# Optimization experiments

Measured on AMD Instinct MI355X. Metric: run time of the kernel, lower is better.

The kernel has to match this reference:

```python
import jax, jax.numpy as jnp
import numpy as np

NEG_SLOPE = 0.2

def _leaky_relu(x):
    return jnp.where(x >= 0, x, NEG_SLOPE * x)


def setup_inputs() -> dict:
    key = jax.random.key(0)
    ks = jax.random.split(key, 8)
    n_s, n_t, nnz = 100000, 20000, 2000000
    d_s_in, d_t_in, d_s_out, d_t_out = 128, 128, 64, 64
    # xavier-uniform-like scale (gain=1.414)
    def xav(k, shape):
        fan_in, fan_out = shape[0], shape[1]
        lim = 1.414 * np.sqrt(6.0 / (fan_in + fan_out))
        return jax.random.uniform(k, shape, jnp.float32, -lim, lim)
    return {
        "x_source": jax.random.normal(ks[0], (n_s, d_s_in), jnp.float32),
        "x_target": jax.random.normal(ks[1], (n_t, d_t_in), jnp.float32),
        "nbhd_values": jax.random.uniform(ks[2], (nnz,), jnp.float32),
        "w_s": xav(ks[3], (d_s_in, d_t_out)),
        "w_t": xav(ks[4], (d_t_in, d_s_out)),
        "att_weight": xav(ks[5], (d_t_out + d_s_out, 1)),
        "row_idx": jax.random.randint(ks[6], (nnz,), 0, n_t),  # target rows of N
        "col_idx": jax.random.randint(ks[7], (nnz,), 0, n_s),  # source cols of N
    }


def reference(x_source, x_target, nbhd_values, w_s, w_t, att_weight, row_idx, col_idx):
    n_s = x_source.shape[0]
    n_t = x_target.shape[0]
    d_t_out = w_s.shape[1]

    s_msg = x_source @ w_s  # [n_s, target_out]
    t_msg = x_target @ w_t  # [n_t, source_out]

    # att_weight applies to concat([s_msg_j, t_msg_i]); split it per-node
    a_s = att_weight[:d_t_out, 0]   # matches s_msg dims
    a_t = att_weight[d_t_out:, 0]   # matches t_msg dims
    s_score = s_msg @ a_s           # [n_s]
    t_score = t_msg @ a_t           # [n_t]

    # per-edge unnormalized attention; identical value for e (N-shaped) and
    # f (N^T-shaped) since concat order + swapped att vector cancel out
    edge = _leaky_relu(s_score[col_idx] + t_score[row_idx])  # [nnz]

    # sparse_row_norm: divide each row by its sum (rows of N for e, rows of N^T for f)
    e_row_sum = jax.ops.segment_sum(edge, row_idx, num_segments=n_t)
    f_row_sum = jax.ops.segment_sum(edge, col_idx, num_segments=n_s)
    e_att = edge / jnp.where(e_row_sum == 0, 1.0, e_row_sum)[row_idx]
    f_att = edge / jnp.where(f_row_sum == 0, 1.0, f_row_sum)[col_idx]

    # Hadamard with neighborhood values, then sparse-dense matmul (scatter-add)
    e_vals = e_att * nbhd_values  # (N \odot A_s) values
    f_vals = f_att * nbhd_values  # (N^T \odot A_t) values
    message_on_target = jax.ops.segment_sum(e_vals[:, None] * s_msg[col_idx], row_idx, num_segments=n_t)
    message_on_source = jax.ops.segment_sum(f_vals[:, None] * t_msg[row_idx], col_idx, num_segments=n_s)

    # update_func=None -> identity
    return message_on_source, message_on_target
```

## Files before the change

kernel.cpp:

```cpp
#include <hip/hip_runtime.h>
#include <stdint.h>

#define D_IN  128
#define D_OUT 64
#define NEG_SLOPE 0.2f
#define SUB       8
#define SUB_SHIFT 3
#define SCAN_CHUNK 4096
#define RPW       8
#define RPB       32

#define CHUNK   2048
#define GS_R    5
#define GS_C    7
#define CAPB_R  3712
#define CAPB_C  3072

__global__ void msg_score8_kernel(const float* __restrict__ x,
                                  const float* __restrict__ w,
                                  const float* __restrict__ att, int att_off,
                                  float* __restrict__ msg,
                                  float* __restrict__ score,
                                  int n_rows) {
    __shared__ float wl[D_IN * D_OUT];
    __shared__ float xs[RPB * D_IN];
    const int tid = threadIdx.x;

    const float4* w4  = (const float4*)w;
    float4*       wl4 = (float4*)wl;
#pragma unroll
    for (int i = 0; i < 8; ++i) wl4[tid + i * 256] = w4[tid + i * 256];

    const int rb = blockIdx.x * RPB;
    float4* xs4 = (float4*)xs;
    const float4* x4 = (const float4*)x;
#pragma unroll
    for (int i = 0; i < 4; ++i) {
        const int f  = tid + i * 256;
        const int r  = f >> 5;
        const int k4 = f & 31;
        const int row = min(rb + r, n_rows - 1);
        xs4[f] = x4[(size_t)row * 32 + k4];
    }
    __syncthreads();

    const int wv = tid >> 6;
    const int j  = tid & 63;
    const int rl = wv * RPW;
    const float4* xw = (const float4*)(xs + rl * D_IN);

    float acc[RPW];
#pragma unroll
    for (int r = 0; r < RPW; ++r) acc[r] = 0.f;

#pragma unroll 2
    for (int k4 = 0; k4 < D_IN / 4; ++k4) {
        const float w0 = wl[(k4 * 4 + 0) * D_OUT + j];
        const float w1 = wl[(k4 * 4 + 1) * D_OUT + j];
        const float w2 = wl[(k4 * 4 + 2) * D_OUT + j];
        const float w3 = wl[(k4 * 4 + 3) * D_OUT + j];
#pragma unroll
        for (int r = 0; r < RPW; ++r) {
            const float4 xv = xw[r * 32 + k4];
            acc[r] += xv.x * w0;
            acc[r] += xv.y * w1;
            acc[r] += xv.z * w2;
            acc[r] += xv.w * w3;
        }
    }

    const float aj = att[att_off + j];
#pragma unroll
    for (int r = 0; r < RPW; ++r) {
        const int row = rb + rl + r;
        if (row < n_rows) msg[(size_t)row * D_OUT + j] = acc[r];
        float v = acc[r] * aj;
#pragma unroll
        for (int off = 32; off > 0; off >>= 1) v += __shfl_down(v, off, 64);
        if (j == 0 && row < n_rows) score[row] = v;
    }
}

__global__ void __launch_bounds__(256)
khist2_kernel(const int* __restrict__ row_idx, const int* __restrict__ col_idx,
              int* __restrict__ cntR, int* __restrict__ cntC,
              int nnz, int ngr, int ngc) {
    extern __shared__ int hs[];
    int* hr = hs;
    int* hc = hs + ngr;
    const int tid  = threadIdx.x;
    const int base = blockIdx.x * CHUNK;
    const int lim  = min(CHUNK, nnz - base);

    for (int k = tid; k < ngr + ngc; k += 256) hs[k] = 0;
    __syncthreads();
    for (int k = tid; k < lim; k += 256) {
        atomicAdd(&hr[row_idx[base + k] >> GS_R], 1);
        atomicAdd(&hc[col_idx[base + k] >> GS_C], 1);
    }
    __syncthreads();
    for (int g = tid; g < ngr; g += 256) cntR[(size_t)blockIdx.x * ngr + g] = hr[g];
    for (int g = tid; g < ngc; g += 256) cntC[(size_t)blockIdx.x * ngc + g] = hc[g];
}

__global__ void __launch_bounds__(256)
kgsum_kernel(const int* __restrict__ cnt, int* __restrict__ gtot,
             int NB, int ng) {
    __shared__ int lds[256];
    const int g = blockIdx.x;
    const int t = threadIdx.x;
    int s = 0;
    for (int b = t; b < NB; b += 256) s += cnt[(size_t)b * ng + g];
    lds[t] = s;
    __syncthreads();
    for (int d = 128; d > 0; d >>= 1) {
        if (t < d) lds[t] += lds[t + d];
        __syncthreads();
    }
    if (t == 0) gtot[g] = lds[0];
}

__global__ void __launch_bounds__(1024)
kgscan2_kernel(const int* __restrict__ gtotR, int* __restrict__ goffR, int ngr,
               const int* __restrict__ gtotC, int* __restrict__ goffC, int ngc) {
    __shared__ int lds[1024];
    const int t = threadIdx.x;
    const int* gt = blockIdx.x ? gtotC : gtotR;
    int*       go = blockIdx.x ? goffC : goffR;
    const int  n  = blockIdx.x ? ngc : ngr;
    const int v = (t < n) ? gt[t] : 0;
    lds[t] = v;
    __syncthreads();
    for (int d = 1; d < 1024; d <<= 1) {
        int u = (t >= d) ? lds[t - d] : 0;
        __syncthreads();
        lds[t] += u;
        __syncthreads();
    }
    if (t < n) go[t] = lds[t] - v;
    if (t == n - 1) go[n] = lds[t];
}

__global__ void __launch_bounds__(256)
kgpos_kernel(const int* __restrict__ cnt, const int* __restrict__ goff,
             int* __restrict__ gpos, int NB, int ng) {
    __shared__ int lds[256];
    const int g = blockIdx.x;
    const int t = threadIdx.x;
    int c[4];
    int s = 0;
#pragma unroll
    for (int u = 0; u < 4; ++u) {
        const int b = 4 * t + u;
        c[u] = (b < NB) ? cnt[(size_t)b * ng + g] : 0;
        s += c[u];
    }
    lds[t] = s;
    __syncthreads();
    for (int d = 1; d < 256; d <<= 1) {
        int u = (t >= d) ? lds[t - d] : 0;
        __syncthreads();
        lds[t] += u;
        __syncthreads();
    }
    int ex = goff[g] + lds[t] - s;
#pragma unroll
    for (int u = 0; u < 4; ++u) {
        const int b = 4 * t + u;
        if (b < NB) { gpos[(size_t)g * NB + b] = ex; ex += c[u]; }
    }
}

__global__ void __launch_bounds__(256)
kpart5_kernel(const int* __restrict__ row_idx,
              const int* __restrict__ col_idx,
              const float* __restrict__ nbhd,
              const float* __restrict__ s_score,
              const float* __restrict__ t_score,
              const int* __restrict__ cntR, const int* __restrict__ cntC,
              const int* __restrict__ gposR, const int* __restrict__ gposC,
              float4* __restrict__ pay_r, float4* __restrict__ pay_c,
              int nnz, int NB, int ngr, int ngc) {
    extern __shared__ char sm[];
    unsigned short* sp = (unsigned short*)sm;
    int* cnt  = (int*)(sm + (size_t)CHUNK * 2);
    int* off  = cnt + (ngc + 1);
    int* gofb = off + (ngc + 1);

    const int tid  = threadIdx.x;
    const int d    = (blockIdx.x >= NB) ? 1 : 0;
    const int b    = blockIdx.x - (d ? NB : 0);
    const int base = b * CHUNK;
    const int lim  = min(CHUNK, nnz - base);

    const int gs   = d ? GS_C : GS_R;
    const int ng   = d ? ngc : ngr;
    const int mask = (1 << gs) - 1;
    const int* kidx = d ? col_idx : row_idx;
    const int* oidx = d ? row_idx : col_idx;
    const int* cp  = d ? cntC : cntR;
    const int* gp  = d ? gposC : gposR;
    float4*    pd  = d ? pay_c : pay_r;

    for (int k = tid; k < ng; k += 256) cnt[k] = cp[(size_t)b * ng + k];
    if (tid == 0) cnt[ng] = 0;
    __syncthreads();

    const int ipt = (ng + 1 + 255) >> 8;
    int c4[4];
    int s = 0;
#pragma unroll
    for (int u = 0; u < 4; ++u) {
        const int k = tid * ipt + u;
        c4[u] = (u < ipt && k <= ng) ? cnt[k] : 0;
        s += c4[u];
    }
    gofb[tid] = s;
    __syncthreads();
    for (int dd = 1; dd < 256; dd <<= 1) {
        const int uu = (tid >= dd) ? gofb[tid - dd] : 0;
        __syncthreads();
        gofb[tid] += uu;
        __syncthreads();
    }
    int ex = gofb[tid] - s;
    __syncthreads();
#pragma unroll
    for (int u = 0; u < 4; ++u) {
        const int k = tid * ipt + u;
        if (u < ipt && k <= ng) { off[k] = ex; cnt[k] = ex; ex += c4[u]; }
    }
    __syncthreads();

    for (int k = tid; k < ng; k += 256) gofb[k] = gp[(size_t)k * NB + b];
    for (int k = tid; k < lim; k += 256) {
        const int grp = kidx[base + k] >> gs;
        const int pos = atomicAdd(&cnt[grp], 1);
        sp[pos] = (unsigned short)k;
    }
    __syncthreads();

    for (int k = tid; k < lim; k += 256) {
        const int t   = sp[k];
        const int key = kidx[base + t];
        const int oth = oidx[base + t];
        const int r   = d ? oth : key;
        const int c   = d ? key : oth;
        const float xv = s_score[c] + t_score[r];
        const float e  = xv >= 0.f ? xv : NEG_SLOPE * xv;
        const int grp = key >> gs;
        pd[(size_t)gofb[grp] + (k - off[grp])] =
            make_float4(__int_as_float(oth | ((key & mask) << 20)),
                        e, nbhd[base + t], 0.f);
    }
}

__global__ void __launch_bounds__(512)
ksort_kernel(float4* __restrict__ pay,
             const int* __restrict__ goff,
             int* __restrict__ koff,
             int kpg, int cap) {
    extern __shared__ char sm[];
    int*    PO   = (int*)sm;
    float*  E    = (float*)(sm + (size_t)cap * 4);
    float*  B    = (float*)(sm + (size_t)cap * 8);
    unsigned short* perm = (unsigned short*)(sm + (size_t)cap * 12);
    int*    scnt = (int*)(sm + (size_t)cap * 14);
    int*    soff = scnt + kpg;
    int*    scur = soff + kpg + 1;

    const int g    = blockIdx.x;
    const int tid  = threadIdx.x;
    const int mask = kpg - 1;

    const int beg = goff[g];
    const int n   = min(goff[g + 1] - beg, cap);

    for (int k = tid; k < kpg; k += 512) scnt[k] = 0;
    __syncthreads();

    for (int k = tid; k < n; k += 512) {
        const float4 p = pay[(size_t)beg + k];
        const int pk = __float_as_int(p.x);
        PO[k] = pk; E[k] = p.y; B[k] = p.z;
        atomicAdd(&scnt[(pk >> 20) & mask], 1);
    }
    __syncthreads();

    if (tid == 0) {
        int a = 0;
        for (int k = 0; k < kpg; ++k) { const int t = scnt[k]; soff[k] = a; scur[k] = a; a += t; }
        soff[kpg] = a;
    }
    __syncthreads();

    for (int k = tid; k < n; k += 512)
        perm[atomicAdd(&scur[(PO[k] >> 20) & mask], 1)] = (unsigned short)k;
    __syncthreads();

    for (int k = tid; k < n; k += 512) {
        const int kk = perm[k];
        pay[(size_t)beg + k] = make_float4(__int_as_float(PO[kk]), E[kk], B[kk], 0.f);
    }
    for (int k = tid; k <= kpg; k += 512)
        koff[(size_t)g * (kpg + 1) + k] = beg + soff[k];
}

__global__ void kaccum2_kernel(const int* __restrict__ koff, int kshift,
                               const float4* __restrict__ pay,
                               const float* __restrict__ other_msg,
                               float* __restrict__ out, int n_mine) {
    const int wave = (int)((blockIdx.x * (size_t)blockDim.x + threadIdx.x) >> 6);
    const int lane = threadIdx.x & 63;
    if (wave >= n_mine) return;

    const int kpg = 1 << kshift;
    const int grp = wave >> kshift;
    const int jk  = wave & (kpg - 1);
    const int beg = koff[(size_t)grp * (kpg + 1) + jk];
    const int end = koff[(size_t)grp * (kpg + 1) + jk + 1];

    double psum = 0.0;
    for (int k = beg + lane; k < end; k += 64) psum += (double)pay[k].y;
#pragma unroll
    for (int o = 32; o > 0; o >>= 1) psum += __shfl_down(psum, o, 64);
    double ers = __shfl(psum, 0, 64);
    if (ers == 0.0) ers = 1.0;
    const double inv = 1.0 / ers;

    const int g = lane >> 4;
    const int q = lane & 15;
    const float4* msg4 = (const float4*)other_msg;
    float4 acc = make_float4(0.f, 0.f, 0.f, 0.f);

    for (int kb = beg; kb < end; kb += 64) {
        const int k = kb + lane;
        int o = 0; float wt = 0.f;
        if (k < end) {
            float4 p = pay[k];
            o  = __float_as_int(p.x) & 0xFFFFF;
            wt = (float)((double)p.y * inv) * p.z;
        }
        const int cnt = min(64, end - kb);
        for (int j = 0; j < cnt; j += 4) {
            const int   jj = j + g;
            const int   oj = __shfl(o,  jj, 64);
            const float wj = __shfl(wt, jj, 64);
            float4 m = msg4[((size_t)oj << 4) + q];
            acc.x += wj * m.x;
            acc.y += wj * m.y;
            acc.z += wj * m.z;
            acc.w += wj * m.w;
        }
    }

#pragma unroll
    for (int d = 16; d < 64; d <<= 1) {
        acc.x += __shfl_xor(acc.x, d, 64);
        acc.y += __shfl_xor(acc.y, d, 64);
        acc.z += __shfl_xor(acc.z, d, 64);
        acc.w += __shfl_xor(acc.w, d, 64);
    }
    if (g == 0) ((float4*)out)[((size_t)wave << 4) + q] = acc;
}

__global__ void hist_kernel(const int* __restrict__ row_idx,
                            const int* __restrict__ col_idx,
                            int* __restrict__ cnt, int col_base, int nnz) {
    const int i = blockIdx.x * blockDim.x + threadIdx.x;
    if (i >= nnz) return;
    const int s = i & (SUB - 1);
    atomicAdd(&cnt[(row_idx[i] << SUB_SHIFT) + s], 1);
    atomicAdd(&cnt[col_base + (col_idx[i] << SUB_SHIFT) + s], 1);
}

__global__ void scan_stage1(const int* __restrict__ cnt, int* __restrict__ bsum,
                            int n) {
    __shared__ int lds[256];
    const int t = threadIdx.x;
    const int base = blockIdx.x * SCAN_CHUNK;
    int s = 0;
    for (int k = t; k < SCAN_CHUNK; k += 256) {
        const int j = base + k;
        if (j < n) s += cnt[j];
    }
    lds[t] = s;
    __syncthreads();
    for (int d = 128; d > 0; d >>= 1) {
        if (t < d) lds[t] += lds[t + d];
        __syncthreads();
    }
    if (t == 0) bsum[blockIdx.x] = lds[0];
}

__global__ void scan_stage2(int* __restrict__ bsum, int nb) {
    __shared__ int lds[1024];
    const int t = threadIdx.x;
    const int v = (t < nb) ? bsum[t] : 0;
    lds[t] = v;
    __syncthreads();
    for (int d = 1; d < 1024; d <<= 1) {
        int u = (t >= d) ? lds[t - d] : 0;
        __syncthreads();
        lds[t] += u;
        __syncthreads();
    }
    if (t < nb) bsum[t] = lds[t] - v;
}

__global__ void scan_stage3(const int* __restrict__ cnt,
                            const int* __restrict__ bsum,
                            int* __restrict__ off, int* __restrict__ cur,
                            int n, int total) {
    __shared__ int lds[256];
    const int t = threadIdx.x;
    const int base = blockIdx.x * SCAN_CHUNK + t * 16;
    int c[16];
    int s = 0;
#pragma unroll
    for (int k = 0; k < 16; ++k) {
        const int j = base + k;
        c[k] = (j < n) ? cnt[j] : 0;
        s += c[k];
    }
    lds[t] = s;
    __syncthreads();
    for (int d = 1; d < 256; d <<= 1) {
        int u = (t >= d) ? lds[t - d] : 0;
        __syncthreads();
        lds[t] += u;
        __syncthreads();
    }
    int ex = bsum[blockIdx.x] + lds[t] - s;
#pragma unroll
    for (int k = 0; k < 16; ++k) {
        const int j = base + k;
        if (j < n) { off[j] = ex; cur[j] = ex; ex += c[k]; }
    }
    if (blockIdx.x == 0 && t == 0) off[n] = total;
}

__global__ void scatter_row_kernel(const int* __restrict__ row_idx,
                                   const int* __restrict__ col_idx,
                                   const float* __restrict__ nbhd,
                                   const float* __restrict__ s_score,
                                   const float* __restrict__ t_score,
                                   int* __restrict__ cur,
                                   float4* __restrict__ pay, int nnz) {
    const int i = blockIdx.x * blockDim.x + threadIdx.x;
    if (i >= nnz) return;
    const int r = row_idx[i];
    const int c = col_idx[i];
    const float xv = s_score[c] + t_score[r];
    const float e  = xv >= 0.f ? xv : NEG_SLOPE * xv;
    const int p = atomicAdd(&cur[(r << SUB_SHIFT) + (i & (SUB - 1))], 1);
    pay[p] = make_float4(__int_as_float(c), e, nbhd[i], 0.f);
}

__global__ void scatter_col_kernel(const int* __restrict__ row_idx,
                                   const int* __restrict__ col_idx,
                                   const float* __restrict__ nbhd,
                                   const float* __restrict__ s_score,
                                   const float* __restrict__ t_score,
                                   int* __restrict__ cur, int col_base,
                                   float4* __restrict__ pay, int nnz) {
    const int i = blockIdx.x * blockDim.x + threadIdx.x;
    if (i >= nnz) return;
    const int r = row_idx[i];
    const int c = col_idx[i];
    const float xv = s_score[c] + t_score[r];
    const float e  = xv >= 0.f ? xv : NEG_SLOPE * xv;
    const int p = atomicAdd(&cur[col_base + (c << SUB_SHIFT) + (i & (SUB - 1))], 1);
    pay[p] = make_float4(__int_as_float(r), e, nbhd[i], 0.f);
}

__global__ void accum_kernel(const int* __restrict__ off, int off_base,
                             const float4* __restrict__ pay,
                             const float* __restrict__ other_msg,
                             float* __restrict__ out, int n_mine) {
    const int wave = (int)((blockIdx.x * (size_t)blockDim.x + threadIdx.x) >> 6);
    const int lane = threadIdx.x & 63;
    if (wave >= n_mine) return;

    const int beg = off[off_base + (wave << SUB_SHIFT)];
    const int end = off[off_base + (wave << SUB_SHIFT) + SUB];

    double psum = 0.0;
    for (int k = beg + lane; k < end; k += 64) psum += (double)pay[k].y;
#pragma unroll
    for (int o = 32; o > 0; o >>= 1) psum += __shfl_down(psum, o, 64);
    double ers = __shfl(psum, 0, 64);
    if (ers == 0.0) ers = 1.0;
    const double inv = 1.0 / ers;

    const int g = lane >> 4;
    const int q = lane & 15;
    const float4* msg4 = (const float4*)other_msg;
    float4 acc = make_float4(0.f, 0.f, 0.f, 0.f);

    for (int kb = beg; kb < end; kb += 64) {
        const int k = kb + lane;
        int o = 0; float wt = 0.f;
        if (k < end) {
            float4 p = pay[k];
            o  = __float_as_int(p.x);
            wt = (float)((double)p.y * inv) * p.z;
        }
        const int cnt = min(64, end - kb);
        for (int j = 0; j < cnt; j += 4) {
            const int   jj = j + g;
            const int   oj = __shfl(o,  jj, 64);
            const float wj = __shfl(wt, jj, 64);
            float4 m = msg4[((size_t)oj << 4) + q];
            acc.x += wj * m.x;
            acc.y += wj * m.y;
            acc.z += wj * m.z;
            acc.w += wj * m.w;
        }
    }

#pragma unroll
    for (int d = 16; d < 64; d <<= 1) {
        acc.x += __shfl_xor(acc.x, d, 64);
        acc.y += __shfl_xor(acc.y, d, 64);
        acc.z += __shfl_xor(acc.z, d, 64);
        acc.w += __shfl_xor(acc.w, d, 64);
    }
    if (g == 0) ((float4*)out)[((size_t)wave << 4) + q] = acc;
}

extern "C" void kernel_launch(void* const* d_in, const int* in_sizes, int n_in,
                              void* d_out, int out_size, void* d_ws, size_t ws_size,
                              hipStream_t stream) {
    const float* x_source = (const float*)d_in[0];
    const float* x_target = (const float*)d_in[1];
    const float* nbhd     = (const float*)d_in[2];
    const float* w_s      = (const float*)d_in[3];
    const float* w_t      = (const float*)d_in[4];
    const float* att      = (const float*)d_in[5];
    const int*   row_idx  = (const int*)d_in[6];
    const int*   col_idx  = (const int*)d_in[7];

    const int n_s = in_sizes[0] / D_IN;
    const int n_t = in_sizes[1] / D_IN;
    const int nnz = in_sizes[2];

    float* out = (float*)d_out;
    float* mos = out;
    float* mot = out + (size_t)n_s * D_OUT;

    char* ws = (char*)d_ws;
    float* s_msg   = (float*)ws;  ws += sizeof(float) * (size_t)n_s * D_OUT;
    float* t_msg   = (float*)ws;  ws += sizeof(float) * (size_t)n_t * D_OUT;
    float* s_score = (float*)ws;  ws += sizeof(float) * (size_t)n_s;
    float* t_score = (float*)ws;  ws += sizeof(float) * (size_t)n_t;

    const int NBCH = (nnz + CHUNK - 1) / CHUNK;
    const int NGR  = (n_t + (1 << GS_R) - 1) >> GS_R;
    const int NGC  = (n_s + (1 << GS_C) - 1) >> GS_C;
    char* wsb = ws;
    int* cntR  = (int*)wsb;  wsb += sizeof(int) * (size_t)NBCH * NGR;
    int* cntC  = (int*)wsb;  wsb += sizeof(int) * (size_t)NBCH * NGC;
    int* gposR = (int*)wsb;  wsb += sizeof(int) * (size_t)NGR * NBCH;
    int* gposC = (int*)wsb;  wsb += sizeof(int) * (size_t)NGC * NBCH;
    int* gtotR = (int*)wsb;  wsb += sizeof(int) * (size_t)NGR;
    int* goffR = (int*)wsb;  wsb += sizeof(int) * (size_t)(NGR + 1);
    int* gtotC = (int*)wsb;  wsb += sizeof(int) * (size_t)NGC;
    int* goffC = (int*)wsb;  wsb += sizeof(int) * (size_t)(NGC + 1);
    int* koffR = (int*)wsb;  wsb += sizeof(int) * (size_t)NGR * ((1 << GS_R) + 1);
    int* koffC = (int*)wsb;  wsb += sizeof(int) * (size_t)NGC * ((1 << GS_C) + 1);
    wsb = (char*)(((uintptr_t)wsb + 15) & ~(uintptr_t)15);
    float4* pay_r = (float4*)wsb;  wsb += sizeof(float4) * (size_t)nnz;
    float4* pay_c = (float4*)wsb;  wsb += sizeof(float4) * (size_t)nnz;
    const size_t need_sort = (size_t)(wsb - (char*)d_ws);

    msg_score8_kernel<<<(n_s + RPB - 1) / RPB, 256, 0, stream>>>(
        x_source, w_s, att, 0, s_msg, s_score, n_s);
    msg_score8_kernel<<<(n_t + RPB - 1) / RPB, 256, 0, stream>>>(
        x_target, w_t, att, D_OUT, t_msg, t_score, n_t);

    if (ws_size >= need_sort) {
        khist2_kernel<<<NBCH, 256, (size_t)(NGR + NGC) * 4, stream>>>(
            row_idx, col_idx, cntR, cntC, nnz, NGR, NGC);

        kgsum_kernel<<<NGR, 256, 0, stream>>>(cntR, gtotR, NBCH, NGR);
        kgsum_kernel<<<NGC, 256, 0, stream>>>(cntC, gtotC, NBCH, NGC);
        kgscan2_kernel<<<2, 1024, 0, stream>>>(gtotR, goffR, NGR, gtotC, goffC, NGC);
        kgpos_kernel<<<NGR, 256, 0, stream>>>(cntR, goffR, gposR, NBCH, NGR);
        kgpos_kernel<<<NGC, 256, 0, stream>>>(cntC, goffC, gposC, NBCH, NGC);

        const size_t smem_part = (size_t)CHUNK * 2 + (size_t)(3 * NGC + 2) * 4;
        kpart5_kernel<<<2 * NBCH, 256, smem_part, stream>>>(
            row_idx, col_idx, nbhd, s_score, t_score,
            cntR, cntC, gposR, gposC, pay_r, pay_c, nnz, NBCH, NGR, NGC);

        const size_t smem_s_r = (size_t)CAPB_R * 14 + (size_t)(3 * (1 << GS_R) + 2) * 4;
        const size_t smem_s_c = (size_t)CAPB_C * 14 + (size_t)(3 * (1 << GS_C) + 2) * 4;
        ksort_kernel<<<NGR, 512, smem_s_r, stream>>>(
            pay_r, goffR, koffR, 1 << GS_R, CAPB_R);
        ksort_kernel<<<NGC, 512, smem_s_c, stream>>>(
            pay_c, goffC, koffC, 1 << GS_C, CAPB_C);

        kaccum2_kernel<<<(int)(((size_t)n_t * 64 + 255) / 256), 256, 0, stream>>>(
            koffR, GS_R, pay_r, s_msg, mot, n_t);
        kaccum2_kernel<<<(int)(((size_t)n_s * 64 + 255) / 256), 256, 0, stream>>>(
            koffC, GS_C, pay_c, t_msg, mos, n_s);
    } else {
        const int col_base = n_t * SUB;
        const int n_cnt    = (n_t + n_s) * SUB;
        const int total    = 2 * nnz;

        char* wsf = ws;
        int* cnt  = (int*)wsf;  wsf += sizeof(int) * (size_t)n_cnt;
        int* cur  = (int*)wsf;  wsf += sizeof(int) * (size_t)n_cnt;
        int* off  = (int*)wsf;  wsf += sizeof(int) * (size_t)(n_cnt + 1);
        int* bsum = (int*)wsf;  wsf += sizeof(int) * 1024;
        wsf = (char*)(((uintptr_t)wsf + 15) & ~(uintptr_t)15);
        float4* pay = (float4*)wsf;

        hipMemsetAsync(cnt, 0, sizeof(int) * (size_t)n_cnt, stream);

        hist_kernel<<<(nnz + 255) / 256, 256, 0, stream>>>(
            row_idx, col_idx, cnt, col_base, nnz);

        const int nb = (n_cnt + SCAN_CHUNK - 1) / SCAN_CHUNK;
        scan_stage1<<<nb, 256, 0, stream>>>(cnt, bsum, n_cnt);
        scan_stage2<<<1, 1024, 0, stream>>>(bsum, nb);
        scan_stage3<<<nb, 256, 0, stream>>>(cnt, bsum, off, cur, n_cnt, total);

        scatter_row_kernel<<<(nnz + 255) / 256, 256, 0, stream>>>(
            row_idx, col_idx, nbhd, s_score, t_score, cur, pay, nnz);
        scatter_col_kernel<<<(nnz + 255) / 256, 256, 0, stream>>>(
            row_idx, col_idx, nbhd, s_score, t_score, cur, col_base, pay, nnz);

        accum_kernel<<<(int)(((size_t)n_t * 64 + 255) / 256), 256, 0, stream>>>(
            off, 0, pay, s_msg, mot, n_t);
        accum_kernel<<<(int)(((size_t)n_s * 64 + 255) / 256), 256, 0, stream>>>(
            off, col_base, pay, t_msg, mos, n_s);
    }
}
```

Baseline: 467.1 us.

## Fuse per-group key sort with attention-weighted accumulation in one kernel

Merges the per-group counting sort and the per-key gather/accumulate into a single kernel. After bucketing in LDS, each wave handles keys of its block directly from shared memory instead of writing the sorted payload back to global memory and rereading it in a separate kernel. This removes a full write and read of the float4 payload arrays, the koff arrays and two launches. In exchange, parallelism drops to one block of 8 waves per group (e.g. 16 keys per wave for the 128-key column groups), so fewer waves are in flight to hide the random message-gather latency, and load imbalance across keys can leave waves idle.

```diff
diff --git a/kernel.cpp b/kernel.cpp
--- a/kernel.cpp
+++ b/kernel.cpp
@@ -256,10 +256,11 @@
 }
 
 __global__ void __launch_bounds__(512)
-ksort_kernel(float4* __restrict__ pay,
-             const int* __restrict__ goff,
-             int* __restrict__ koff,
-             int kpg, int cap) {
+kaccum3_kernel(const float4* __restrict__ pay,
+               const int* __restrict__ goff,
+               const float* __restrict__ other_msg,
+               float* __restrict__ out,
+               int kpg, int n_keys, int cap) {
     extern __shared__ char sm[];
     int*    PO   = (int*)sm;
     float*  E    = (float*)(sm + (size_t)cap * 4);
@@ -298,70 +299,58 @@
         perm[atomicAdd(&scur[(PO[k] >> 20) & mask], 1)] = (unsigned short)k;
     __syncthreads();
 
-    for (int k = tid; k < n; k += 512) {
-        const int kk = perm[k];
-        pay[(size_t)beg + k] = make_float4(__int_as_float(PO[kk]), E[kk], B[kk], 0.f);
-    }
-    for (int k = tid; k <= kpg; k += 512)
-        koff[(size_t)g * (kpg + 1) + k] = beg + soff[k];
-}
-
-__global__ void kaccum2_kernel(const int* __restrict__ koff, int kshift,
-                               const float4* __restrict__ pay,
-                               const float* __restrict__ other_msg,
-                               float* __restrict__ out, int n_mine) {
-    const int wave = (int)((blockIdx.x * (size_t)blockDim.x + threadIdx.x) >> 6);
-    const int lane = threadIdx.x & 63;
-    if (wave >= n_mine) return;
-
-    const int kpg = 1 << kshift;
-    const int grp = wave >> kshift;
-    const int jk  = wave & (kpg - 1);
-    const int beg = koff[(size_t)grp * (kpg + 1) + jk];
-    const int end = koff[(size_t)grp * (kpg + 1) + jk + 1];
-
-    double psum = 0.0;
-    for (int k = beg + lane; k < end; k += 64) psum += (double)pay[k].y;
-#pragma unroll
-    for (int o = 32; o > 0; o >>= 1) psum += __shfl_down(psum, o, 64);
-    double ers = __shfl(psum, 0, 64);
-    if (ers == 0.0) ers = 1.0;
-    const double inv = 1.0 / ers;
-
-    const int g = lane >> 4;
-    const int q = lane & 15;
+    const int wv   = tid >> 6;
+    const int lane = tid & 63;
+    const int gg = lane >> 4;
+    const int q  = lane & 15;
     const float4* msg4 = (const float4*)other_msg;
-    float4 acc = make_float4(0.f, 0.f, 0.f, 0.f);
-
-    for (int kb = beg; kb < end; kb += 64) {
-        const int k = kb + lane;
-        int o = 0; float wt = 0.f;
-        if (k < end) {
-            float4 p = pay[k];
-            o  = __float_as_int(p.x) & 0xFFFFF;
-            wt = (float)((double)p.y * inv) * p.z;
+
+    for (int lr = wv; lr < kpg; lr += 8) {
+        const int key = g * kpg + lr;
+        if (key >= n_keys) continue;
+        const int b2  = soff[lr];
+        const int end = soff[lr + 1];
+
+        double psum = 0.0;
+        for (int k = b2 + lane; k < end; k += 64) psum += (double)E[perm[k]];
+#pragma unroll
+        for (int o = 32; o > 0; o >>= 1) psum += __shfl_down(psum, o, 64);
+        double ers = __shfl(psum, 0, 64);
+        if (ers == 0.0) ers = 1.0;
+        const double inv = 1.0 / ers;
+
+        float4 acc = make_float4(0.f, 0.f, 0.f, 0.f);
+        for (int kb = b2; kb < end; kb += 64) {
+            const int k = kb + lane;
+            int o = 0; float wt = 0.f;
+            if (k < end) {
+                const int kk = perm[k];
+                o  = PO[kk] & 0xFFFFF;
+                wt = (float)((double)E[kk] * inv) * B[kk];
+            }
+            const int cnt2 = min(64, end - kb);
+            for (int j = 0; j < cnt2; j += 4) {
+                const int   jj = j + gg;
+                const int   oj = __shfl(o,  jj, 64);
+                const float wj = __shfl(wt, jj, 64);
+                const float4 m = msg4[((size_t)oj << 4) + q];
+                acc.x += wj * m.x;
+                acc.y += wj * m.y;
+                acc.z += wj * m.z;
+                acc.w += wj * m.w;
+            }
         }
-        const int cnt = min(64, end - kb);
-        for (int j = 0; j < cnt; j += 4) {
-            const int   jj = j + g;
-            const int   oj = __shfl(o,  jj, 64);
-            const float wj = __shfl(wt, jj, 64);
-            float4 m = msg4[((size_t)oj << 4) + q];
-            acc.x += wj * m.x;
-            acc.y += wj * m.y;
-            acc.z += wj * m.z;
-            acc.w += wj * m.w;
+
+#pragma unroll
+        for (int d = 16; d < 64; d <<= 1) {
+            acc.x += __shfl_xor(acc.x, d, 64);
+            acc.y += __shfl_xor(acc.y, d, 64);
+            acc.z += __shfl_xor(acc.z, d, 64);
+            acc.w += __shfl_xor(acc.w, d, 64);
         }
-    }
-
-#pragma unroll
-    for (int d = 16; d < 64; d <<= 1) {
-        acc.x += __shfl_xor(acc.x, d, 64);
-        acc.y += __shfl_xor(acc.y, d, 64);
-        acc.z += __shfl_xor(acc.z, d, 64);
-        acc.w += __shfl_xor(acc.w, d, 64);
-    }
-    if (g == 0) ((float4*)out)[((size_t)wave << 4) + q] = acc;
+        if (gg == 0)
+            ((float4*)out)[((size_t)key << 4) + q] = acc;
+    }
 }
 
 __global__ void hist_kernel(const int* __restrict__ row_idx,
@@ -567,8 +556,6 @@
     int* goffR = (int*)wsb;  wsb += sizeof(int) * (size_t)(NGR + 1);
     int* gtotC = (int*)wsb;  wsb += sizeof(int) * (size_t)NGC;
     int* goffC = (int*)wsb;  wsb += sizeof(int) * (size_t)(NGC + 1);
-    int* koffR = (int*)wsb;  wsb += sizeof(int) * (size_t)NGR * ((1 << GS_R) + 1);
-    int* koffC = (int*)wsb;  wsb += sizeof(int) * (size_t)NGC * ((1 << GS_C) + 1);
     wsb = (char*)(((uintptr_t)wsb + 15) & ~(uintptr_t)15);
     float4* pay_r = (float4*)wsb;  wsb += sizeof(float4) * (size_t)nnz;
     float4* pay_c = (float4*)wsb;  wsb += sizeof(float4) * (size_t)nnz;
@@ -594,17 +581,12 @@
             row_idx, col_idx, nbhd, s_score, t_score,
             cntR, cntC, gposR, gposC, pay_r, pay_c, nnz, NBCH, NGR, NGC);
 
-        const size_t smem_s_r = (size_t)CAPB_R * 14 + (size_t)(3 * (1 << GS_R) + 2) * 4;
-        const size_t smem_s_c = (size_t)CAPB_C * 14 + (size_t)(3 * (1 << GS_C) + 2) * 4;
-        ksort_kernel<<<NGR, 512, smem_s_r, stream>>>(
-            pay_r, goffR, koffR, 1 << GS_R, CAPB_R);
-        ksort_kernel<<<NGC, 512, smem_s_c, stream>>>(
-            pay_c, goffC, koffC, 1 << GS_C, CAPB_C);
-
-        kaccum2_kernel<<<(int)(((size_t)n_t * 64 + 255) / 256), 256, 0, stream>>>(
-            koffR, GS_R, pay_r, s_msg, mot, n_t);
-        kaccum2_kernel<<<(int)(((size_t)n_s * 64 + 255) / 256), 256, 0, stream>>>(
-            koffC, GS_C, pay_c, t_msg, mos, n_s);
+        const size_t smem_a_r = (size_t)CAPB_R * 14 + (size_t)(3 * (1 << GS_R) + 2) * 4;
+        const size_t smem_a_c = (size_t)CAPB_C * 14 + (size_t)(3 * (1 << GS_C) + 2) * 4;
+        kaccum3_kernel<<<NGR, 512, smem_a_r, stream>>>(
+            pay_r, goffR, s_msg, mot, 1 << GS_R, n_t, CAPB_R);
+        kaccum3_kernel<<<NGC, 512, smem_a_c, stream>>>(
+            pay_c, goffC, t_msg, mos, 1 << GS_C, n_s, CAPB_C);
     } else {
         const int col_base = n_t * SUB;
         const int n_cnt    = (n_t + n_s) * SUB;
```

Result: slower. 480.7 us (+2.9%).
